# Performance work log

Hardware: AMD Instinct MI355X
Metric: run time of the kernel (lower is better)

Reference implementation:

```python
import jax, jax.numpy as jnp
import numpy as np

C = 384      # c_s
NF = 16      # n_freq
H = 256      # mlp_hidden
B, K, N = 4, 2048, 16384
POS_WEIGHT = 1.5  # not used; see below


def _ln(x, g, b, eps=1e-5):
    m = x.mean(-1, keepdims=True)
    v = ((x - m) ** 2).mean(-1, keepdims=True)
    return (x - m) * jax.lax.rsqrt(v + eps) * g + b


def setup_inputs() -> dict:
    key = jax.random.key(0)
    ks = jax.random.split(key, 24)
    w = lambda k, shp: (jax.random.normal(k, shp, jnp.float32) * 0.02)
    inp = {
        "s_parent": jax.random.normal(ks[0], (B, K, C), jnp.float32),
        "mu_k": jax.random.normal(ks[1], (B, K, 3), jnp.float32),
        "R_k": jax.random.normal(ks[2], (B, K, 3, 3), jnp.float32),
        "s_k": jax.random.uniform(ks[3], (B, K, 3), jnp.float32),
        "a_idx": jax.random.randint(ks[4], (B, N), 0, K, jnp.int32),
        "node_mask": jnp.ones((B, N), jnp.float32),
        "pos01": jax.random.uniform(ks[5], (B, N), jnp.float32),
        # Pos01FourierEncoder: Linear(2*NF -> C)
        "pos_w": w(ks[6], (C, 2 * NF)), "pos_b": jnp.zeros((C,), jnp.float32),
        # q_proj: LayerNorm(C), Linear(C,C), SiLU, Linear(C,C)
        "q_ln_g": jnp.ones((C,), jnp.float32), "q_ln_b": jnp.zeros((C,), jnp.float32),
        "q_w1": w(ks[7], (C, C)), "q_b1": jnp.zeros((C,), jnp.float32),
        "q_w2": w(ks[8], (C, C)), "q_b2": jnp.zeros((C,), jnp.float32),
        # mlp: LayerNorm(C), Linear(C,H), SiLU, Linear(H,H), SiLU, Linear(H,3)
        "m_ln_g": jnp.ones((C,), jnp.float32), "m_ln_b": jnp.zeros((C,), jnp.float32),
        "m_w1": w(ks[9], (H, C)), "m_b1": jnp.zeros((H,), jnp.float32),
        "m_w2": w(ks[10], (H, H)), "m_b2": jnp.zeros((H,), jnp.float32),
        "m_w3": w(ks[11], (3, H)), "m_b3": jnp.zeros((3,), jnp.float32),
    }
    return inp


def reference(s_parent, mu_k, R_k, s_k, a_idx, node_mask, pos01,
              pos_w, pos_b, q_ln_g, q_ln_b, q_w1, q_b1, q_w2, q_b2,
              m_ln_g, m_ln_b, m_w1, m_b1, m_w2, m_b2, m_w3, m_b3):
    pos_weight = 1.0
    scale = 1.5
    mask = node_mask[..., None]  # [B,N,1]

    # Fourier positional encoding of pos01 in [0,1]
    freqs = (2.0 ** jnp.arange(NF, dtype=jnp.float32)) * np.float32(np.pi)
    ang = pos01[..., None] * freqs                          # [B,N,NF]
    feats = jnp.concatenate([jnp.sin(ang), jnp.cos(ang)], -1)  # [B,N,2NF]
    pos_emb = (feats @ pos_w.T + pos_b) * mask              # [B,N,C]

    idx = jnp.clip(a_idx, 0, K - 1)
    s_pi = jnp.take_along_axis(s_parent, idx[:, :, None], axis=1)  # [B,N,C]
    s_pi = s_pi + pos_weight * pos_emb

    # q_proj
    q = _ln(s_pi, q_ln_g, q_ln_b)
    q = jax.nn.silu(q @ q_w1.T + q_b1)
    q = (q @ q_w2.T + q_b2) * mask

    # mlp -> xi_hat
    h = _ln(q, m_ln_g, m_ln_b)
    h = jax.nn.silu(h @ m_w1.T + m_b1)
    h = jax.nn.silu(h @ m_w2.T + m_b2)
    xi = (h @ m_w3.T + m_b3) * mask
    xi_hat = jnp.tanh(xi) * scale                           # [B,N,3]

    # gather parent rigid params per node
    mu_i = jnp.take_along_axis(mu_k, idx[:, :, None], axis=1)            # [B,N,3]
    s_i = jnp.take_along_axis(jnp.maximum(s_k, 1e-8), idx[:, :, None], axis=1)
    R_i = jnp.take_along_axis(R_k, idx[:, :, None, None], axis=1)        # [B,N,3,3]

    # rigid apply: x = R @ (xi * s) + mu
    x_hat = jnp.einsum('bnij,bnj->bni', R_i, xi_hat * s_i) + mu_i
    x_hat = x_hat * mask
    return xi_hat, x_hat * 10.0, pos01
```

## Files before the change

kernel.cpp:

```cpp
#include <hip/hip_runtime.h>
#include <hip/hip_bf16.h>
#include <math.h>

#define C 384
#define NF 16
#define H 256
#define Bb 4
#define Kk 2048
#define Nn 16384
#define MB 64
#define LDA 392

typedef __attribute__((ext_vector_type(8))) short bf16x8;
typedef __attribute__((ext_vector_type(4))) float f32x4;
typedef __attribute__((ext_vector_type(4))) short s16x4;

#define POS_OFF 0
#define Q1_OFF  12288
#define Q2_OFF  159744
#define M1_OFF  307200
#define M2_OFF  405504
#define M3_OFF  471040
#define W_TOTAL 475136

__device__ __attribute__((always_inline)) inline short f2bf(float x) {
    return __builtin_bit_cast(short, __float2bfloat16(x));
}
__device__ __attribute__((always_inline)) inline float bf2f(short s) {
    return __bfloat162float(__builtin_bit_cast(__hip_bfloat16, s));
}
__device__ __attribute__((always_inline)) inline float silu(float v) {
    return v * __builtin_amdgcn_rcpf(1.f + __expf(-v));
}

__global__ __launch_bounds__(256) void conv_w(
    const float* __restrict__ pos_w, const float* __restrict__ q_w1,
    const float* __restrict__ q_w2,  const float* __restrict__ m_w1,
    const float* __restrict__ m_w2,  const float* __restrict__ m_w3,
    short* __restrict__ ws)
{
    int i = blockIdx.x * 256 + threadIdx.x;
    if (i >= W_TOTAL) return;
    const float* src; int off, K;
    if      (i < Q1_OFF) { src = pos_w; off = POS_OFF; K = 32; }
    else if (i < Q2_OFF) { src = q_w1;  off = Q1_OFF;  K = 384; }
    else if (i < M1_OFF) { src = q_w2;  off = Q2_OFF;  K = 384; }
    else if (i < M2_OFF) { src = m_w1;  off = M1_OFF;  K = 384; }
    else if (i < M3_OFF) { src = m_w2;  off = M2_OFF;  K = 256; }
    else                 { src = m_w3;  off = M3_OFF;  K = 256; }
    int t = i - off;
    int chunk = t >> 9, r = t & 511;
    int ln = r >> 5, kq = r & 31;
    int NKm = K >> 5;
    int ntg = chunk / NKm, kk = chunk - ntg * NKm;
    int f = ntg * 16 + ln, k = kk * 32 + kq;
    float v;
    if (off == M3_OFF) v = (f < 3) ? m_w3[f * 256 + k] : 0.f;
    else               v = src[(size_t)f * K + k];
    ws[i] = f2bf(v);
}

__device__ __attribute__((always_inline)) inline void ln_apply(
    short (*__restrict__ xs)[LDA], const float* __restrict__ g,
    const float* __restrict__ bb,
    float (*__restrict__ sc1)[4], float (*__restrict__ sc2)[4], int tid)
{
    int m = tid >> 2, j = tid & 3;
    float s1 = sc1[m][0] + sc1[m][1] + sc1[m][2] + sc1[m][3];
    float s2 = sc2[m][0] + sc2[m][1] + sc2[m][2] + sc2[m][3];
    float mean = s1 * (1.f / 384.f);
    float var  = s2 * (1.f / 384.f) - mean * mean;
    float rstd = rsqrtf(var + 1e-5f);
    int c0 = j * 96;
    #pragma unroll
    for (int i = 0; i < 12; ++i) {
        int cc = c0 + i * 8;
        bf16x8 v8 = *(bf16x8*)&xs[m][cc];
        bf16x8 o8;
        #pragma unroll
        for (int e = 0; e < 8; ++e) {
            float v = (bf2f(v8[e]) - mean) * rstd * g[cc + e] + bb[cc + e];
            o8[e] = f2bf(v);
        }
        *(bf16x8*)&xs[m][cc] = o8;
    }
}

template<int K, int NT, int NTN, int KN, bool SILU_, bool MASK, bool STATS>
__device__ __attribute__((always_inline)) inline void layer_ip(
    const short* __restrict__ W, const float* __restrict__ bias, int FB,
    const short* __restrict__ Wn, int FBn,
    bf16x8 (&bin)[6],
    short (*__restrict__ xs)[LDA],
    float (*__restrict__ sc1)[4], float (*__restrict__ sc2)[4],
    const float* __restrict__ wmask, int w, int q, int ln)
{
    constexpr int NK = K / 32;
    const short* bp[NT];
    #pragma unroll
    for (int nt = 0; nt < NT; ++nt)
        bp[nt] = W + ((size_t)(FB / 16 + nt) * NK) * 512 + ln * 32 + q * 8;

    f32x4 acc[4][NT];
    #pragma unroll
    for (int mt = 0; mt < 4; ++mt)
        #pragma unroll
        for (int nt = 0; nt < NT; ++nt)
            acc[mt][nt] = (f32x4){0.f, 0.f, 0.f, 0.f};

    bf16x8 b0[NT], b1[NT], a0[4], a1[4];
    #pragma unroll
    for (int nt = 0; nt < NT; ++nt) b0[nt] = bin[nt];
    #pragma unroll
    for (int mt = 0; mt < 4; ++mt) a0[mt] = *(const bf16x8*)&xs[mt * 16 + ln][q * 8];

    #pragma unroll
    for (int kc = 0; kc < NK; kc += 2) {
        #pragma unroll
        for (int nt = 0; nt < NT; ++nt) b1[nt] = *(const bf16x8*)(bp[nt] + (kc + 1) * 512);
        #pragma unroll
        for (int mt = 0; mt < 4; ++mt) a1[mt] = *(const bf16x8*)&xs[mt * 16 + ln][(kc + 1) * 32 + q * 8];
        #pragma unroll
        for (int nt = 0; nt < NT; ++nt)
            #pragma unroll
            for (int mt = 0; mt < 4; ++mt)
                acc[mt][nt] = __builtin_amdgcn_mfma_f32_16x16x32_bf16(b0[nt], a0[mt], acc[mt][nt], 0, 0, 0);
        if (kc + 2 < NK) {
            #pragma unroll
            for (int nt = 0; nt < NT; ++nt) b0[nt] = *(const bf16x8*)(bp[nt] + (kc + 2) * 512);
            #pragma unroll
            for (int mt = 0; mt < 4; ++mt) a0[mt] = *(const bf16x8*)&xs[mt * 16 + ln][(kc + 2) * 32 + q * 8];
        }
        #pragma unroll
        for (int nt = 0; nt < NT; ++nt)
            #pragma unroll
            for (int mt = 0; mt < 4; ++mt)
                acc[mt][nt] = __builtin_amdgcn_mfma_f32_16x16x32_bf16(b1[nt], a1[mt], acc[mt][nt], 0, 0, 0);
    }

    #pragma unroll
    for (int nt = 0; nt < NTN; ++nt)
        bin[nt] = *(const bf16x8*)(Wn + ((size_t)(FBn / 16 + nt) * (KN / 32)) * 512 + ln * 32 + q * 8);

    __syncthreads();

    float mk[4];
    #pragma unroll
    for (int mt = 0; mt < 4; ++mt) mk[mt] = wmask[mt * 16 + ln];

    float s1[4] = {0.f,0.f,0.f,0.f}, s2[4] = {0.f,0.f,0.f,0.f};
    #pragma unroll
    for (int nt = 0; nt < NT; ++nt) {
        const int f0 = FB + nt * 16 + q * 4;
        f32x4 bv = *(const f32x4*)&bias[f0];
        #pragma unroll
        for (int mt = 0; mt < 4; ++mt) {
            s16x4 o4;
            #pragma unroll
            for (int r = 0; r < 4; ++r) {
                float v = acc[mt][nt][r] + bv[r];
                if (SILU_) v = silu(v);
                if (MASK) v *= mk[mt];
                if (STATS) { s1[mt] += v; s2[mt] += v * v; }
                o4[r] = f2bf(v);
            }
            *(s16x4*)&xs[mt * 16 + ln][f0] = o4;
        }
    }
    if (STATS) {
        #pragma unroll
        for (int mt = 0; mt < 4; ++mt) {
            s1[mt] += __shfl_xor(s1[mt], 16); s2[mt] += __shfl_xor(s2[mt], 16);
            s1[mt] += __shfl_xor(s1[mt], 32); s2[mt] += __shfl_xor(s2[mt], 32);
        }
        if (q == 0) {
            #pragma unroll
            for (int mt = 0; mt < 4; ++mt) {
                sc1[mt * 16 + ln][w] = s1[mt];
                sc2[mt * 16 + ln][w] = s2[mt];
            }
        }
    }
    __syncthreads();
}

__global__ __launch_bounds__(256, 2) void upxi64(
    const float* __restrict__ s_parent, const float* __restrict__ mu_k,
    const float* __restrict__ R_k,      const float* __restrict__ s_k,
    const int*   __restrict__ a_idx,    const float* __restrict__ node_mask,
    const float* __restrict__ pos01,
    const float* __restrict__ pos_b,
    const float* __restrict__ q_ln_g,   const float* __restrict__ q_ln_b,
    const float* __restrict__ q_b1,     const float* __restrict__ q_b2,
    const float* __restrict__ m_ln_g,   const float* __restrict__ m_ln_b,
    const float* __restrict__ m_b1,     const float* __restrict__ m_b2,
    const float* __restrict__ m_b3,
    const short* __restrict__ wsb,
    float* __restrict__ out)
{
    __shared__ short xs[MB][LDA];
    __shared__ float sc1[MB][4];
    __shared__ float sc2[MB][4];
    __shared__ float wmask[MB], wpos[MB];
    __shared__ int   widx[MB];

    const int tid  = threadIdx.x;
    const int w    = tid >> 6;
    const int lane = tid & 63;
    const int q    = lane >> 4;
    const int ln   = lane & 15;

    const int g0 = blockIdx.x * MB;
    const int b  = g0 / Nn;
    const int n0 = g0 % Nn;

    bf16x8 bin[6];
    #pragma unroll
    for (int nt = 0; nt < 6; ++nt)
        bin[nt] = *(const bf16x8*)(wsb + Q1_OFF + ((size_t)(w * 6 + nt) * 12) * 512 + ln * 32 + q * 8);

    if (tid < MB) {
        int gi = b * Nn + n0 + tid;
        int idx = a_idx[gi];
        widx[tid]  = min(max(idx, 0), Kk - 1);
        wmask[tid] = node_mask[gi];
        wpos[tid]  = pos01[gi];
    }
    __syncthreads();

    const float* gbase = s_parent + (long)b * Kk * C;

    {
        const short* pos_wb = wsb + POS_OFF;
        const bool use_sin = (q < 2);
        const int kb = (q & 1) * 8;
        bf16x8 a[4];
        #pragma unroll
        for (int mt = 0; mt < 4; ++mt) {
            float p = wpos[mt * 16 + ln];
            #pragma unroll
            for (int e = 0; e < 8; ++e) {
                float fr = (float)(1 << (kb + e)) * 3.14159265358979323846f;
                float sv, cv;
                __sincosf(p * fr, &sv, &cv);
                a[mt][e] = f2bf(use_sin ? sv : cv);
            }
        }
        f32x4 acc[4][6];
        #pragma unroll
        for (int mt = 0; mt < 4; ++mt)
            #pragma unroll
            for (int nt = 0; nt < 6; ++nt)
                acc[mt][nt] = (f32x4){0.f, 0.f, 0.f, 0.f};
        #pragma unroll
        for (int nt = 0; nt < 6; ++nt) {
            bf16x8 bfr = *(const bf16x8*)&pos_wb[(w * 6 + nt) * 512 + ln * 32 + q * 8];
            #pragma unroll
            for (int mt = 0; mt < 4; ++mt)
                acc[mt][nt] = __builtin_amdgcn_mfma_f32_16x16x32_bf16(bfr, a[mt], acc[mt][nt], 0, 0, 0);
        }
        float mk[4]; int ix[4];
        #pragma unroll
        for (int mt = 0; mt < 4; ++mt) {
            mk[mt] = wmask[mt * 16 + ln];
            ix[mt] = widx[mt * 16 + ln];
        }
        float s1[4] = {0.f,0.f,0.f,0.f}, s2[4] = {0.f,0.f,0.f,0.f};
        #pragma unroll
        for (int nt = 0; nt < 6; ++nt) {
            const int f0 = w * 96 + nt * 16 + q * 4;
            f32x4 pb4 = *(const f32x4*)&pos_b[f0];
            #pragma unroll
            for (int mt = 0; mt < 4; ++mt) {
                f32x4 g4 = *(const f32x4*)&gbase[(long)ix[mt] * C + f0];
                s16x4 o4;
                #pragma unroll
                for (int r = 0; r < 4; ++r) {
                    float v = (acc[mt][nt][r] + pb4[r]) * mk[mt] + g4[r];
                    s1[mt] += v; s2[mt] += v * v;
                    o4[r] = f2bf(v);
                }
                *(s16x4*)&xs[mt * 16 + ln][f0] = o4;
            }
        }
        #pragma unroll
        for (int mt = 0; mt < 4; ++mt) {
            s1[mt] += __shfl_xor(s1[mt], 16); s2[mt] += __shfl_xor(s2[mt], 16);
            s1[mt] += __shfl_xor(s1[mt], 32); s2[mt] += __shfl_xor(s2[mt], 32);
        }
        if (q == 0) {
            #pragma unroll
            for (int mt = 0; mt < 4; ++mt) {
                sc1[mt * 16 + ln][w] = s1[mt];
                sc2[mt * 16 + ln][w] = s2[mt];
            }
        }
    }
    __syncthreads();

    ln_apply(xs, q_ln_g, q_ln_b, sc1, sc2, tid);
    __syncthreads();

    layer_ip<384, 6, 6, 384, true,  false, false>(wsb + Q1_OFF, q_b1, w * 96,
        wsb + Q2_OFF, w * 96, bin, xs, sc1, sc2, wmask, w, q, ln);
    layer_ip<384, 6, 4, 384, false, true,  true >(wsb + Q2_OFF, q_b2, w * 96,
        wsb + M1_OFF, w * 64, bin, xs, sc1, sc2, wmask, w, q, ln);

    ln_apply(xs, m_ln_g, m_ln_b, sc1, sc2, tid);
    __syncthreads();

    layer_ip<384, 4, 4, 256, true, false, false>(wsb + M1_OFF, m_b1, w * 64,
        wsb + M2_OFF, w * 64, bin, xs, sc1, sc2, wmask, w, q, ln);
    layer_ip<256, 4, 1, 256, true, false, false>(wsb + M2_OFF, m_b2, w * 64,
        wsb + M3_OFF, 0, bin, xs, sc1, sc2, wmask, w, q, ln);

    {
        const short* W3 = wsb + M3_OFF;
        f32x4 a3 = (f32x4){0.f, 0.f, 0.f, 0.f};
        #pragma unroll
        for (int kc = 0; kc < 8; ++kc) {
            bf16x8 a  = *(const bf16x8*)&xs[w * 16 + ln][kc * 32 + q * 8];
            bf16x8 bf = (kc == 0) ? bin[0]
                      : *(const bf16x8*)(W3 + kc * 512 + ln * 32 + q * 8);
            a3 = __builtin_amdgcn_mfma_f32_16x16x32_bf16(bf, a, a3, 0, 0, 0);
        }
        if (q == 0) {
            int m = w * 16 + ln;
            float mkv = wmask[m];
            #pragma unroll
            for (int r = 0; r < 3; ++r) {
                float v = (a3[r] + m_b3[r]) * mkv;
                sc1[m][r] = tanhf(v) * 1.5f;
            }
        }
    }

    if (lane < 16) {
        int m = w * 16 + lane;
        long gi = (long)b * Nn + n0 + m;
        long pk = (long)b * Kk + widx[m];
        float mkv = wmask[m];
        float xv[3], yv[3], xiv[3];
        #pragma unroll
        for (int j = 0; j < 3; ++j) {
            xiv[j] = sc1[m][j];
            float sc = fmaxf(s_k[pk * 3 + j], 1e-8f);
            xv[j] = xiv[j] * sc;
        }
        #pragma unroll
        for (int i = 0; i < 3; ++i) {
            float a = R_k[pk * 9 + i * 3 + 0] * xv[0]
                    + R_k[pk * 9 + i * 3 + 1] * xv[1]
                    + R_k[pk * 9 + i * 3 + 2] * xv[2]
                    + mu_k[pk * 3 + i];
            yv[i] = a * mkv * 10.f;
        }
        float* o0 = out;
        float* o1 = out + (long)Bb * Nn * 3;
        float* o2 = out + (long)Bb * Nn * 6;
        #pragma unroll
        for (int j = 0; j < 3; ++j) { o0[gi * 3 + j] = xiv[j]; o1[gi * 3 + j] = yv[j]; }
        o2[gi] = wpos[m];
    }
}

extern "C" void kernel_launch(void* const* d_in, const int* in_sizes, int n_in,
                              void* d_out, int out_size, void* d_ws, size_t ws_size,
                              hipStream_t stream) {
    const float* s_parent = (const float*)d_in[0];
    const float* mu_k     = (const float*)d_in[1];
    const float* R_k      = (const float*)d_in[2];
    const float* s_k      = (const float*)d_in[3];
    const int*   a_idx    = (const int*)  d_in[4];
    const float* node_mask= (const float*)d_in[5];
    const float* pos01    = (const float*)d_in[6];
    const float* pos_w    = (const float*)d_in[7];
    const float* pos_b    = (const float*)d_in[8];
    const float* q_ln_g   = (const float*)d_in[9];
    const float* q_ln_b   = (const float*)d_in[10];
    const float* q_w1     = (const float*)d_in[11];
    const float* q_b1     = (const float*)d_in[12];
    const float* q_w2     = (const float*)d_in[13];
    const float* q_b2     = (const float*)d_in[14];
    const float* m_ln_g   = (const float*)d_in[15];
    const float* m_ln_b   = (const float*)d_in[16];
    const float* m_w1     = (const float*)d_in[17];
    const float* m_b1     = (const float*)d_in[18];
    const float* m_w2     = (const float*)d_in[19];
    const float* m_b2     = (const float*)d_in[20];
    const float* m_w3     = (const float*)d_in[21];
    const float* m_b3     = (const float*)d_in[22];

    short* wsb = (short*)d_ws;

    conv_w<<<(W_TOTAL + 255) / 256, 256, 0, stream>>>(
        pos_w, q_w1, q_w2, m_w1, m_w2, m_w3, wsb);

    int blocks = (Bb * Nn) / MB;
    upxi64<<<blocks, 256, 0, stream>>>(
        s_parent, mu_k, R_k, s_k, a_idx, node_mask, pos01,
        pos_b, q_ln_g, q_ln_b, q_b1, q_b2,
        m_ln_g, m_ln_b, m_b1, m_b2, m_b3,
        wsb, (float*)d_out);
}
```

Measured before the change: 226.4 us.

## Fold LayerNorm affine into following linear weights and apply normalization in epilogue

Folds the LayerNorm gamma into the bf16 weights of the following linear layers and precomputes per-output constants (weight row sums and beta/bias terms) in a small setup kernel. Each GEMM then runs on the raw activations, and its epilogue applies rstd*acc - rstd*mean*G + c. This removes the separate in-shared-memory LN pass and its barrier before two of the layers. The trade-offs are an extra kernel launch, some epilogue arithmetic, and slightly different rounding, since the GEMM input is no longer normalized before the bf16 conversion.

After: 208.0 us. -8.1%, faster.

```diff
diff --git a/kernel.cpp b/kernel.cpp
--- a/kernel.cpp
+++ b/kernel.cpp
@@ -22,6 +22,10 @@
 #define M2_OFF  405504
 #define M3_OFF  471040
 #define W_TOTAL 475136
+#define GQ_OFF 0
+#define CQ_OFF 384
+#define GM_OFF 768
+#define CM_OFF 1024
 
 __device__ __attribute__((always_inline)) inline short f2bf(float x) {
     return __builtin_bit_cast(short, __float2bfloat16(x));
@@ -37,6 +41,7 @@
     const float* __restrict__ pos_w, const float* __restrict__ q_w1,
     const float* __restrict__ q_w2,  const float* __restrict__ m_w1,
     const float* __restrict__ m_w2,  const float* __restrict__ m_w3,
+    const float* __restrict__ q_ln_g, const float* __restrict__ m_ln_g,
     short* __restrict__ ws)
 {
     int i = blockIdx.x * 256 + threadIdx.x;
@@ -57,38 +62,45 @@
     float v;
     if (off == M3_OFF) v = (f < 3) ? m_w3[f * 256 + k] : 0.f;
     else               v = src[(size_t)f * K + k];
+    if (off == Q1_OFF) v *= q_ln_g[k];
+    if (off == M1_OFF) v *= m_ln_g[k];
     ws[i] = f2bf(v);
 }
 
-__device__ __attribute__((always_inline)) inline void ln_apply(
-    short (*__restrict__ xs)[LDA], const float* __restrict__ g,
-    const float* __restrict__ bb,
-    float (*__restrict__ sc1)[4], float (*__restrict__ sc2)[4], int tid)
+__global__ __launch_bounds__(256) void fold_consts(
+    const float* __restrict__ q_w1, const float* __restrict__ q_b1,
+    const float* __restrict__ q_ln_g, const float* __restrict__ q_ln_b,
+    const float* __restrict__ m_w1, const float* __restrict__ m_b1,
+    const float* __restrict__ m_ln_g, const float* __restrict__ m_ln_b,
+    float* __restrict__ cst)
 {
-    int m = tid >> 2, j = tid & 3;
-    float s1 = sc1[m][0] + sc1[m][1] + sc1[m][2] + sc1[m][3];
-    float s2 = sc2[m][0] + sc2[m][1] + sc2[m][2] + sc2[m][3];
-    float mean = s1 * (1.f / 384.f);
-    float var  = s2 * (1.f / 384.f) - mean * mean;
-    float rstd = rsqrtf(var + 1e-5f);
-    int c0 = j * 96;
-    #pragma unroll
-    for (int i = 0; i < 12; ++i) {
-        int cc = c0 + i * 8;
-        bf16x8 v8 = *(bf16x8*)&xs[m][cc];
-        bf16x8 o8;
-        #pragma unroll
-        for (int e = 0; e < 8; ++e) {
-            float v = (bf2f(v8[e]) - mean) * rstd * g[cc + e] + bb[cc + e];
-            o8[e] = f2bf(v);
-        }
-        *(bf16x8*)&xs[m][cc] = o8;
-    }
-}
-
-template<int K, int NT, int NTN, int KN, bool SILU_, bool MASK, bool STATS>
+    int f = blockIdx.x * 256 + threadIdx.x;
+    if (f < 384) {
+        float g = 0.f, c = 0.f;
+        for (int k = 0; k < 384; ++k) {
+            float w = q_w1[(size_t)f * 384 + k];
+            g += bf2f(f2bf(w * q_ln_g[k]));
+            c += w * q_ln_b[k];
+        }
+        cst[GQ_OFF + f] = g;
+        cst[CQ_OFF + f] = c + q_b1[f];
+    } else if (f < 640) {
+        int f2 = f - 384;
+        float g = 0.f, c = 0.f;
+        for (int k = 0; k < 384; ++k) {
+            float w = m_w1[(size_t)f2 * 384 + k];
+            g += bf2f(f2bf(w * m_ln_g[k]));
+            c += w * m_ln_b[k];
+        }
+        cst[GM_OFF + f2] = g;
+        cst[CM_OFF + f2] = c + m_b1[f2];
+    }
+}
+
+template<int K, int NT, int NTN, int KN, bool SILU_, bool MASK, bool LNIN, bool STATS>
 __device__ __attribute__((always_inline)) inline void layer_ip(
-    const short* __restrict__ W, const float* __restrict__ bias, int FB,
+    const short* __restrict__ W, const float* __restrict__ cb,
+    const float* __restrict__ Gf, int FB,
     const short* __restrict__ Wn, int FBn,
     bf16x8 (&bin)[6],
     short (*__restrict__ xs)[LDA],
@@ -144,21 +156,38 @@
 
     __syncthreads();
 
-    float mk[4];
-    #pragma unroll
-    for (int mt = 0; mt < 4; ++mt) mk[mt] = wmask[mt * 16 + ln];
+    float mk[4], rstd[4], rm[4];
+    #pragma unroll
+    for (int mt = 0; mt < 4; ++mt) {
+        int m = mt * 16 + ln;
+        if (MASK) mk[mt] = wmask[m];
+        if (LNIN) {
+            f32x4 p1 = *(const f32x4*)&sc1[m][0];
+            f32x4 p2 = *(const f32x4*)&sc2[m][0];
+            float t1 = p1[0] + p1[1] + p1[2] + p1[3];
+            float t2 = p2[0] + p2[1] + p2[2] + p2[3];
+            float mean = t1 * (1.f / 384.f);
+            float var  = t2 * (1.f / 384.f) - mean * mean;
+            rstd[mt] = rsqrtf(var + 1e-5f);
+            rm[mt]   = rstd[mt] * mean;
+        }
+    }
 
     float s1[4] = {0.f,0.f,0.f,0.f}, s2[4] = {0.f,0.f,0.f,0.f};
     #pragma unroll
     for (int nt = 0; nt < NT; ++nt) {
         const int f0 = FB + nt * 16 + q * 4;
-        f32x4 bv = *(const f32x4*)&bias[f0];
+        f32x4 c4 = *(const f32x4*)&cb[f0];
+        f32x4 g4;
+        if (LNIN) g4 = *(const f32x4*)&Gf[f0];
         #pragma unroll
         for (int mt = 0; mt < 4; ++mt) {
             s16x4 o4;
             #pragma unroll
             for (int r = 0; r < 4; ++r) {
-                float v = acc[mt][nt][r] + bv[r];
+                float v;
+                if (LNIN) v = fmaf(rstd[mt], acc[mt][nt][r], fmaf(-rm[mt], g4[r], c4[r]));
+                else      v = acc[mt][nt][r] + c4[r];
                 if (SILU_) v = silu(v);
                 if (MASK) v *= mk[mt];
                 if (STATS) { s1[mt] += v; s2[mt] += v * v; }
@@ -190,12 +219,9 @@
     const int*   __restrict__ a_idx,    const float* __restrict__ node_mask,
     const float* __restrict__ pos01,
     const float* __restrict__ pos_b,
-    const float* __restrict__ q_ln_g,   const float* __restrict__ q_ln_b,
-    const float* __restrict__ q_b1,     const float* __restrict__ q_b2,
-    const float* __restrict__ m_ln_g,   const float* __restrict__ m_ln_b,
-    const float* __restrict__ m_b1,     const float* __restrict__ m_b2,
+    const float* __restrict__ q_b2,     const float* __restrict__ m_b2,
     const float* __restrict__ m_b3,
-    const short* __restrict__ wsb,
+    const short* __restrict__ wsb,      const float* __restrict__ cst,
     float* __restrict__ out)
 {
     __shared__ short xs[MB][LDA];
@@ -298,21 +324,14 @@
     }
     __syncthreads();
 
-    ln_apply(xs, q_ln_g, q_ln_b, sc1, sc2, tid);
-    __syncthreads();
-
-    layer_ip<384, 6, 6, 384, true,  false, false>(wsb + Q1_OFF, q_b1, w * 96,
-        wsb + Q2_OFF, w * 96, bin, xs, sc1, sc2, wmask, w, q, ln);
-    layer_ip<384, 6, 4, 384, false, true,  true >(wsb + Q2_OFF, q_b2, w * 96,
-        wsb + M1_OFF, w * 64, bin, xs, sc1, sc2, wmask, w, q, ln);
-
-    ln_apply(xs, m_ln_g, m_ln_b, sc1, sc2, tid);
-    __syncthreads();
-
-    layer_ip<384, 4, 4, 256, true, false, false>(wsb + M1_OFF, m_b1, w * 64,
-        wsb + M2_OFF, w * 64, bin, xs, sc1, sc2, wmask, w, q, ln);
-    layer_ip<256, 4, 1, 256, true, false, false>(wsb + M2_OFF, m_b2, w * 64,
-        wsb + M3_OFF, 0, bin, xs, sc1, sc2, wmask, w, q, ln);
+    layer_ip<384, 6, 6, 384, true,  false, true,  false>(wsb + Q1_OFF, cst + CQ_OFF,
+        cst + GQ_OFF, w * 96, wsb + Q2_OFF, w * 96, bin, xs, sc1, sc2, wmask, w, q, ln);
+    layer_ip<384, 6, 4, 384, false, true,  false, true >(wsb + Q2_OFF, q_b2,
+        nullptr, w * 96, wsb + M1_OFF, w * 64, bin, xs, sc1, sc2, wmask, w, q, ln);
+    layer_ip<384, 4, 4, 256, true,  false, true,  false>(wsb + M1_OFF, cst + CM_OFF,
+        cst + GM_OFF, w * 64, wsb + M2_OFF, w * 64, bin, xs, sc1, sc2, wmask, w, q, ln);
+    layer_ip<256, 4, 1, 256, true,  false, false, false>(wsb + M2_OFF, m_b2,
+        nullptr, w * 64, wsb + M3_OFF, 0, bin, xs, sc1, sc2, wmask, w, q, ln);
 
     {
         const short* W3 = wsb + M3_OFF;
@@ -392,14 +411,15 @@
     const float* m_b3     = (const float*)d_in[22];
 
     short* wsb = (short*)d_ws;
+    float* cst = (float*)(wsb + W_TOTAL);
 
     conv_w<<<(W_TOTAL + 255) / 256, 256, 0, stream>>>(
-        pos_w, q_w1, q_w2, m_w1, m_w2, m_w3, wsb);
+        pos_w, q_w1, q_w2, m_w1, m_w2, m_w3, q_ln_g, m_ln_g, wsb);
+    fold_consts<<<3, 256, 0, stream>>>(
+        q_w1, q_b1, q_ln_g, q_ln_b, m_w1, m_b1, m_ln_g, m_ln_b, cst);
 
     int blocks = (Bb * Nn) / MB;
     upxi64<<<blocks, 256, 0, stream>>>(
         s_parent, mu_k, R_k, s_k, a_idx, node_mask, pos01,
-        pos_b, q_ln_g, q_ln_b, q_b1, q_b2,
-        m_ln_g, m_ln_b, m_b1, m_b2, m_b3,
-        wsb, (float*)d_out);
-}
+        pos_b, q_b2, m_b2, m_b3, wsb, cst, (float*)d_out);
+}
```
